# Kernel optimization log

Measured on AMD Instinct MI355X. Metric: run time of the kernel, lower is better.

The kernel has to match this reference:

```python
import jax, jax.numpy as jnp
import numpy as np
import math

B, S, HID = 2, 2048, 1024
NH, HD = 16, 64  # num_heads, head_dim = HID // NH


def setup_inputs() -> dict:
    key = jax.random.key(0)
    ks = jax.random.split(key, 12)
    sc = 1.0 / math.sqrt(HID)
    inp = {
        "x": jax.random.normal(ks[0], (B, S, HID), dtype=jnp.float32),
        "time_deltas": jax.random.uniform(ks[1], (B, S), dtype=jnp.float32),
        # torch.nn.Linear weights are [out, in]; y = x @ W.T + b
        "Wq": jax.random.normal(ks[2], (HID, HID), dtype=jnp.float32) * sc,
        "bq": jnp.zeros((HID,), dtype=jnp.float32),
        "Wk": jax.random.normal(ks[3], (HID, HID), dtype=jnp.float32) * sc,
        "bk": jnp.zeros((HID,), dtype=jnp.float32),
        "Wv": jax.random.normal(ks[4], (HID, HID), dtype=jnp.float32) * sc,
        "bv": jnp.zeros((HID,), dtype=jnp.float32),
        "Wo": jax.random.normal(ks[5], (HID, HID), dtype=jnp.float32) * sc,
        "bo": jnp.zeros((HID,), dtype=jnp.float32),
        "time_decay": jnp.ones((NH,), dtype=jnp.float32),
    }
    return inp


def reference(x, time_deltas, Wq, bq, Wk, bk, Wv, bv, Wo, bo, time_decay):
    b, s, _ = x.shape

    def heads(W, bias):
        # [b, s, hid] -> [b, nh, s, hd]
        return (x @ W.T + bias).reshape(b, s, NH, HD).transpose(0, 2, 1, 3)

    q = heads(Wq, bq)
    k = heads(Wk, bk)
    v = heads(Wv, bv)

    scores = jnp.einsum("bhqd,bhkd->bhqk", q, k) / math.sqrt(HD)

    # pairwise |t_i - t_j| decay bias, per-head learned rate
    tm = jnp.abs(time_deltas[:, :, None] - time_deltas[:, None, :])  # [b, s, s]
    decay = jnp.exp(-time_decay[None, :, None, None] * tm[:, None, :, :])
    scores = scores * decay

    causal = jnp.triu(jnp.ones((s, s), dtype=bool), k=1)  # True above diagonal
    scores = jnp.where(causal[None, None], -jnp.inf, scores)

    attn = jax.nn.softmax(scores, axis=-1)  # dropout is identity at inference
    out = jnp.einsum("bhqk,bhkd->bhqd", attn, v)
    out = out.transpose(0, 2, 1, 3).reshape(b, s, HID)
    return out @ Wo.T + bo
```

## Files before the change

### kernel.cpp

```cpp
#include <hip/hip_runtime.h>
#include <hip/hip_bf16.h>

typedef __attribute__((ext_vector_type(4))) float f32x4;
typedef __attribute__((ext_vector_type(8))) __bf16 bf16x8;
typedef __attribute__((ext_vector_type(4))) unsigned short us4;

static constexpr int BB = 2, SS = 2048, HID = 1024, NH = 16, HD = 64;
static constexpr int M_TOT = BB * SS;

static __device__ __forceinline__ f32x4 mfma16(bf16x8 a, bf16x8 b, f32x4 c) {
  return __builtin_amdgcn_mfma_f32_16x16x32_bf16(a, b, c, 0, 0, 0);
}

static __device__ __forceinline__ unsigned short f2b(float x) {
  __hip_bfloat16 h = __float2bfloat16(x);
  unsigned short u;
  __builtin_memcpy(&u, &h, 2);
  return u;
}

static __device__ __forceinline__ float ex2(float x) {
  return __builtin_amdgcn_exp2f(x);
}

__global__ void cvt_kernel(const float* __restrict__ src,
                           unsigned short* __restrict__ dst, int n4) {
  int idx = blockIdx.x * blockDim.x + threadIdx.x;
  int stride = gridDim.x * blockDim.x;
  const f32x4* s = (const f32x4*)src;
  us4* d = (us4*)dst;
  for (int i = idx; i < n4; i += stride) {
    f32x4 v = s[i];
    us4 o;
    o.x = f2b(v.x); o.y = f2b(v.y); o.z = f2b(v.z); o.w = f2b(v.w);
    d[i] = o;
  }
}

__global__ void cvt_w4(const float* __restrict__ s0, const float* __restrict__ s1,
                       const float* __restrict__ s2, const float* __restrict__ s3,
                       unsigned short* __restrict__ d0, unsigned short* __restrict__ d1,
                       unsigned short* __restrict__ d2, unsigned short* __restrict__ d3,
                       int n4) {
  const float* s; unsigned short* d;
  int z = blockIdx.y;
  if (z == 0)      { s = s0; d = d0; }
  else if (z == 1) { s = s1; d = d1; }
  else if (z == 2) { s = s2; d = d2; }
  else             { s = s3; d = d3; }
  int idx = blockIdx.x * blockDim.x + threadIdx.x;
  int stride = gridDim.x * blockDim.x;
  const f32x4* sv = (const f32x4*)s;
  us4* dv = (us4*)d;
  for (int i = idx; i < n4; i += stride) {
    f32x4 v = sv[i];
    us4 o;
    o.x = f2b(v.x); o.y = f2b(v.y); o.z = f2b(v.z); o.w = f2b(v.w);
    dv[i] = o;
  }
}

static __device__ __forceinline__ void gemm_mainloop(
    const unsigned short* __restrict__ gA,
    const unsigned short* __restrict__ gB,
    unsigned short* As, unsigned short* Bs, int t, f32x4 acc[4][4]) {
  const int l = t & 63;
  const int lr = l & 15, lg = (l >> 4) & 3;
  const int w = t >> 6;
  const int wr = w >> 1, wc = w & 1;
  for (int k0 = 0; k0 < HID; k0 += 64) {
#pragma unroll
    for (int i_ = 0; i_ < 4; ++i_) {
      int chunk = i_ * 256 + t;
      int row = chunk >> 3;
      int col = (chunk & 7) << 3;
      __builtin_amdgcn_global_load_lds(
          (const __attribute__((address_space(1))) unsigned int*)(gA + (size_t)row * HID + k0 + col),
          (__attribute__((address_space(3))) unsigned int*)(As + chunk * 8),
          16, 0, 0);
    }
#pragma unroll
    for (int i_ = 0; i_ < 4; ++i_) {
      int chunk = i_ * 256 + t;
      int row = chunk >> 3;
      int col = (chunk & 7) << 3;
      __builtin_amdgcn_global_load_lds(
          (const __attribute__((address_space(1))) unsigned int*)(gB + (size_t)row * HID + k0 + col),
          (__attribute__((address_space(3))) unsigned int*)(Bs + chunk * 8),
          16, 0, 0);
    }
    __syncthreads();
#pragma unroll
    for (int kk = 0; kk < 2; ++kk) {
      bf16x8 a[4], bb[4];
#pragma unroll
      for (int mf = 0; mf < 4; ++mf)
        a[mf] = *(const bf16x8*)&As[(wr * 64 + mf * 16 + lr) * 64 + kk * 32 + lg * 8];
#pragma unroll
      for (int nf = 0; nf < 4; ++nf)
        bb[nf] = *(const bf16x8*)&Bs[(wc * 64 + nf * 16 + lr) * 64 + kk * 32 + lg * 8];
#pragma unroll
      for (int mf = 0; mf < 4; ++mf)
#pragma unroll
        for (int nf = 0; nf < 4; ++nf)
          acc[mf][nf] = mfma16(a[mf], bb[nf], acc[mf][nf]);
    }
    __syncthreads();
  }
}

__global__ __launch_bounds__(256, 2) void qkv_gemm(
    const unsigned short* __restrict__ xb,
    const unsigned short* __restrict__ wqb, const unsigned short* __restrict__ wkb,
    const unsigned short* __restrict__ wvb,
    const float* __restrict__ bq, const float* __restrict__ bk, const float* __restrict__ bv,
    unsigned short* __restrict__ qo, unsigned short* __restrict__ ko,
    unsigned short* __restrict__ vto) {
  __shared__ unsigned short As[128 * 64];
  __shared__ unsigned short Bs[128 * 64];
  int t = threadIdx.x;
  int z = blockIdx.z;
  const unsigned short* Bmat = (z == 0) ? wqb : (z == 1) ? wkb : wvb;
  const float* bias = (z == 0) ? bq : (z == 1) ? bk : bv;
  int m0 = blockIdx.y * 128, n0 = blockIdx.x * 128;
  f32x4 acc[4][4] = {};
  gemm_mainloop(xb + (size_t)m0 * HID, Bmat + (size_t)n0 * HID, As, Bs, t, acc);

  int l = t & 63, lr = l & 15, lg = (l >> 4) & 3;
  int w = t >> 6, wr = w >> 1, wc = w & 1;
  float scale = (z == 0) ? 0.125f : 1.0f;
#pragma unroll
  for (int nf = 0; nf < 4; ++nf) {
    int n = n0 + wc * 64 + nf * 16 + lr;
    float bs = bias[n];
    int h = n >> 6, d = n & 63;
#pragma unroll
    for (int mf = 0; mf < 4; ++mf) {
#pragma unroll
      for (int j = 0; j < 4; ++j) {
        int m = m0 + wr * 64 + mf * 16 + lg * 4 + j;
        int b = m >> 11, sidx = m & (SS - 1);
        float val = (acc[mf][nf][j] + bs) * scale;
        unsigned short ob = f2b(val);
        if (z == 2)
          vto[((size_t)(b * NH + h) * HD + d) * SS + sidx] = ob;
        else {
          unsigned short* dst = (z == 0) ? qo : ko;
          dst[((size_t)(b * NH + h) * SS + sidx) * HD + d] = ob;
        }
      }
    }
  }
}

__global__ __launch_bounds__(256, 2) void out_gemm(
    const unsigned short* __restrict__ Ab,
    const unsigned short* __restrict__ Wb,
    const float* __restrict__ bias,
    float* __restrict__ C) {
  __shared__ unsigned short As[128 * 64];
  __shared__ unsigned short Bs[128 * 64];
  int t = threadIdx.x;
  int m0 = blockIdx.y * 128, n0 = blockIdx.x * 128;
  f32x4 acc[4][4] = {};
  gemm_mainloop(Ab + (size_t)m0 * HID, Wb + (size_t)n0 * HID, As, Bs, t, acc);

  int l = t & 63, lr = l & 15, lg = (l >> 4) & 3;
  int w = t >> 6, wr = w >> 1, wc = w & 1;
#pragma unroll
  for (int nf = 0; nf < 4; ++nf) {
    int n = n0 + wc * 64 + nf * 16 + lr;
    float bs = bias[n];
#pragma unroll
    for (int mf = 0; mf < 4; ++mf) {
#pragma unroll
      for (int j = 0; j < 4; ++j) {
        int m = m0 + wr * 64 + mf * 16 + lg * 4 + j;
        C[(size_t)m * HID + n] = acc[mf][nf][j] + bs;
      }
    }
  }
}

static __device__ __forceinline__ void stage_kv(
    const unsigned short* __restrict__ kp, const unsigned short* __restrict__ vp,
    int kv0, unsigned short* Kd, unsigned short* Vd, int t) {
#pragma unroll
  for (int i_ = 0; i_ < 2; ++i_) {
    int chunk = i_ * 256 + t;
    int row = chunk >> 3;
    int srcc = ((chunk & 7) ^ (row & 7)) << 3;
    __builtin_amdgcn_global_load_lds(
        (const __attribute__((address_space(1))) unsigned int*)(kp + (size_t)(kv0 + row) * HD + srcc),
        (__attribute__((address_space(3))) unsigned int*)(Kd + chunk * 8), 16, 0, 0);
    __builtin_amdgcn_global_load_lds(
        (const __attribute__((address_space(1))) unsigned int*)(vp + (size_t)row * SS + kv0 + srcc),
        (__attribute__((address_space(3))) unsigned int*)(Vd + chunk * 8), 16, 0, 0);
  }
}

__global__ __launch_bounds__(256, 2) void attn_kernel(
    const unsigned short* __restrict__ qg,
    const unsigned short* __restrict__ kg,
    const unsigned short* __restrict__ vtg,
    const float* __restrict__ td,
    const float* __restrict__ decay,
    unsigned short* __restrict__ outb) {
  __shared__ unsigned short Ks[2][64 * 64];
  __shared__ unsigned short Vs[2][64 * 64];
  __shared__ unsigned short Pl[4][16][64];
  const int t = threadIdx.x;
  const int l = t & 63;
  const int w = t >> 6;
  const int lr = l & 15, lg = (l >> 4) & 3;
  const int L = blockIdx.x;
  const int W = (L & 7) * 64 + (L >> 3);
  const int xp = W & 15;
  const int h = (W >> 4) & 15;
  const int b = W >> 8;
  const unsigned short* qp = qg + ((size_t)(b * NH + h) * SS) * HD;
  const unsigned short* kp = kg + ((size_t)(b * NH + h) * SS) * HD;
  const unsigned short* vp = vtg + ((size_t)(b * NH + h) * HD) * SS;
  const float* tdb = td + (size_t)b * SS;
  const float dec = decay[h];
  const float L2E = 1.44269504f;
  const float dl = dec * L2E;
  const float SHIFT = 16.0f;

  for (int seg = 0; seg < 2; ++seg) {
    const int qb = seg ? 31 - xp : xp;
    const int q0 = qb * 64;
    const int qw = q0 + w * 16;

    bf16x8 qf0 = *(const bf16x8*)&qp[(size_t)(qw + lr) * HD + lg * 8];
    bf16x8 qf1 = *(const bf16x8*)&qp[(size_t)(qw + lr) * HD + 32 + lg * 8];
    float eqL[4], fqL[4];
#pragma unroll
    for (int j = 0; j < 4; ++j) {
      float tq = tdb[qw + lg * 4 + j];
      eqL[j] = ex2(dl * tq) * L2E;
      fqL[j] = ex2(-dl * tq) * L2E;
    }
    float lsum[4] = {0.f, 0.f, 0.f, 0.f};
    f32x4 o[4] = {};

    stage_kv(kp, vp, 0, Ks[0], Vs[0], t);
    int cur = 0;
    for (int tkv = 0; tkv <= qb; ++tkv) {
      const int kv0 = tkv * 64;
      if (tkv < qb) {
        stage_kv(kp, vp, kv0 + 64, Ks[cur ^ 1], Vs[cur ^ 1], t);
        asm volatile("s_waitcnt vmcnt(4)" ::: "memory");
      } else {
        asm volatile("s_waitcnt vmcnt(0)" ::: "memory");
      }
      __builtin_amdgcn_s_barrier();
      asm volatile("" ::: "memory");
      const unsigned short* Kc = Ks[cur];
      const unsigned short* Vc = Vs[cur];

      f32x4 s[4];
#pragma unroll
      for (int nf = 0; nf < 4; ++nf) {
        int r = nf * 16 + lr;
        bf16x8 kf0 = *(const bf16x8*)&Kc[r * 64 + ((lg ^ (r & 7)) << 3)];
        bf16x8 kf1 = *(const bf16x8*)&Kc[r * 64 + (((4 + lg) ^ (r & 7)) << 3)];
        f32x4 zz = {};
        zz = mfma16(qf0, kf0, zz);
        s[nf] = mfma16(qf1, kf1, zz);
      }
      const bool diag = (tkv == qb);
#pragma unroll
      for (int nf = 0; nf < 4; ++nf) {
        int col = kv0 + nf * 16 + lr;
        float tk = tdb[col];
        float ek = ex2(dl * tk);
        float fk = ex2(-dl * tk);
#pragma unroll
        for (int j = 0; j < 4; ++j) {
          int row = lg * 4 + j;
          float wL = fminf(eqL[j] * fk, fqL[j] * ek);
          float pv = ex2(s[nf][j] * wL - SHIFT);
          if (diag && col > qw + row) pv = 0.f;
          lsum[j] += pv;
          Pl[w][row][(nf * 16 + lr) ^ ((row & 7) << 3)] = f2b(pv);
        }
      }
#pragma unroll
      for (int kk = 0; kk < 2; ++kk) {
        bf16x8 pa = *(const bf16x8*)&Pl[w][lr][(kk * 32 + lg * 8) ^ ((lr & 7) << 3)];
        int g = kk * 4 + lg;
#pragma unroll
        for (int df = 0; df < 4; ++df) {
          int r = df * 16 + lr;
          bf16x8 vf = *(const bf16x8*)&Vc[r * 64 + ((g ^ (r & 7)) << 3)];
          o[df] = mfma16(pa, vf, o[df]);
        }
      }
      __syncthreads();
      cur ^= 1;
    }
#pragma unroll
    for (int j = 0; j < 4; ++j) {
      float rs = lsum[j];
      rs += __shfl_xor(rs, 1, 16);
      rs += __shfl_xor(rs, 2, 16);
      rs += __shfl_xor(rs, 4, 16);
      rs += __shfl_xor(rs, 8, 16);
      float inv = 1.0f / rs;
      int srow = qw + lg * 4 + j;
#pragma unroll
      for (int df = 0; df < 4; ++df)
        outb[((size_t)b * SS + srow) * HID + h * HD + df * 16 + lr] = f2b(o[df][j] * inv);
    }
  }
}

extern "C" void kernel_launch(void* const* d_in, const int* in_sizes, int n_in,
                              void* d_out, int out_size, void* d_ws, size_t ws_size,
                              hipStream_t stream) {
  const float* x    = (const float*)d_in[0];
  const float* td   = (const float*)d_in[1];
  const float* Wq   = (const float*)d_in[2];
  const float* bq   = (const float*)d_in[3];
  const float* Wk   = (const float*)d_in[4];
  const float* bk   = (const float*)d_in[5];
  const float* Wv   = (const float*)d_in[6];
  const float* bv   = (const float*)d_in[7];
  const float* Wo   = (const float*)d_in[8];
  const float* bo   = (const float*)d_in[9];
  const float* tdec = (const float*)d_in[10];
  float* out = (float*)d_out;

  char* ws = (char*)d_ws;
  unsigned short* xb  = (unsigned short*)ws; ws += (size_t)M_TOT * HID * 2;
  unsigned short* wqb = (unsigned short*)ws; ws += (size_t)HID * HID * 2;
  unsigned short* wkb = (unsigned short*)ws; ws += (size_t)HID * HID * 2;
  unsigned short* wvb = (unsigned short*)ws; ws += (size_t)HID * HID * 2;
  unsigned short* wob = (unsigned short*)ws; ws += (size_t)HID * HID * 2;
  unsigned short* qb  = (unsigned short*)ws; ws += (size_t)M_TOT * HID * 2;
  unsigned short* kb  = (unsigned short*)ws; ws += (size_t)M_TOT * HID * 2;
  unsigned short* vtb = (unsigned short*)ws; ws += (size_t)M_TOT * HID * 2;
  unsigned short* ob  = (unsigned short*)ws; ws += (size_t)M_TOT * HID * 2;

  cvt_kernel<<<1024, 256, 0, stream>>>(x, xb, M_TOT * HID / 4);
  cvt_w4<<<dim3(512, 4), 256, 0, stream>>>(Wq, Wk, Wv, Wo, wqb, wkb, wvb, wob, HID * HID / 4);
  qkv_gemm<<<dim3(HID / 128, M_TOT / 128, 3), 256, 0, stream>>>(
      xb, wqb, wkb, wvb, bq, bk, bv, qb, kb, vtb);
  attn_kernel<<<512, 256, 0, stream>>>(qb, kb, vtb, td, tdec, ob);
  out_gemm<<<dim3(HID / 128, M_TOT / 128), 256, 0, stream>>>(ob, wob, bo, out);
}
```

Measured before the change: 210.8 us.

## Double-buffer GEMM LDS tiles and merge conversion kernels into one launch

The shared GEMM mainloop now prefetches the next K tile into a second LDS buffer via global_load_lds while computing on the current one, using explicit vmcnt waits and raw barriers instead of __syncthreads. LDS per block doubles to 64 KB, which may limit occupancy for the two-blocks-per-CU launch bound. The separate x and weight fp32-to-bf16 conversion kernels are merged into a single launch with a 5-row grid to save one kernel launch. The x slice now gets 512 blocks instead of 1024, so the larger conversion has less parallelism.

After: 227.6 us. +8.0%, slower.

```diff
diff --git a/kernel.cpp b/kernel.cpp
--- a/kernel.cpp
+++ b/kernel.cpp
@@ -23,31 +23,19 @@
   return __builtin_amdgcn_exp2f(x);
 }
 
-__global__ void cvt_kernel(const float* __restrict__ src,
-                           unsigned short* __restrict__ dst, int n4) {
-  int idx = blockIdx.x * blockDim.x + threadIdx.x;
-  int stride = gridDim.x * blockDim.x;
-  const f32x4* s = (const f32x4*)src;
-  us4* d = (us4*)dst;
-  for (int i = idx; i < n4; i += stride) {
-    f32x4 v = s[i];
-    us4 o;
-    o.x = f2b(v.x); o.y = f2b(v.y); o.z = f2b(v.z); o.w = f2b(v.w);
-    d[i] = o;
-  }
-}
-
-__global__ void cvt_w4(const float* __restrict__ s0, const float* __restrict__ s1,
-                       const float* __restrict__ s2, const float* __restrict__ s3,
-                       unsigned short* __restrict__ d0, unsigned short* __restrict__ d1,
-                       unsigned short* __restrict__ d2, unsigned short* __restrict__ d3,
-                       int n4) {
-  const float* s; unsigned short* d;
-  int z = blockIdx.y;
-  if (z == 0)      { s = s0; d = d0; }
-  else if (z == 1) { s = s1; d = d1; }
-  else if (z == 2) { s = s2; d = d2; }
-  else             { s = s3; d = d3; }
+__global__ void cvt_all(const float* __restrict__ x,  const float* __restrict__ wq,
+                        const float* __restrict__ wk, const float* __restrict__ wv,
+                        const float* __restrict__ wo,
+                        unsigned short* __restrict__ xb,  unsigned short* __restrict__ wqb,
+                        unsigned short* __restrict__ wkb, unsigned short* __restrict__ wvb,
+                        unsigned short* __restrict__ wob) {
+  int y = blockIdx.y;
+  const float* s; unsigned short* d; int n4;
+  if (y == 0)      { s = x;  d = xb;  n4 = M_TOT * HID / 4; }
+  else if (y == 1) { s = wq; d = wqb; n4 = HID * HID / 4; }
+  else if (y == 2) { s = wk; d = wkb; n4 = HID * HID / 4; }
+  else if (y == 3) { s = wv; d = wvb; n4 = HID * HID / 4; }
+  else             { s = wo; d = wob; n4 = HID * HID / 4; }
   int idx = blockIdx.x * blockDim.x + threadIdx.x;
   int stride = gridDim.x * blockDim.x;
   const f32x4* sv = (const f32x4*)s;
@@ -60,52 +48,63 @@
   }
 }
 
+static __device__ __forceinline__ void stage_ab(
+    const unsigned short* __restrict__ gA, const unsigned short* __restrict__ gB,
+    int k0, unsigned short* As, unsigned short* Bs, int t) {
+#pragma unroll
+  for (int i_ = 0; i_ < 4; ++i_) {
+    int chunk = i_ * 256 + t;
+    int row = chunk >> 3;
+    int col = (chunk & 7) << 3;
+    __builtin_amdgcn_global_load_lds(
+        (const __attribute__((address_space(1))) unsigned int*)(gA + (size_t)row * HID + k0 + col),
+        (__attribute__((address_space(3))) unsigned int*)(As + chunk * 8), 16, 0, 0);
+    __builtin_amdgcn_global_load_lds(
+        (const __attribute__((address_space(1))) unsigned int*)(gB + (size_t)row * HID + k0 + col),
+        (__attribute__((address_space(3))) unsigned int*)(Bs + chunk * 8), 16, 0, 0);
+  }
+}
+
 static __device__ __forceinline__ void gemm_mainloop(
     const unsigned short* __restrict__ gA,
     const unsigned short* __restrict__ gB,
-    unsigned short* As, unsigned short* Bs, int t, f32x4 acc[4][4]) {
+    unsigned short* As, unsigned short* Bs,
+    int t, f32x4 acc[4][4]) {
   const int l = t & 63;
   const int lr = l & 15, lg = (l >> 4) & 3;
   const int w = t >> 6;
   const int wr = w >> 1, wc = w & 1;
+  stage_ab(gA, gB, 0, As, Bs, t);
+  int cur = 0;
   for (int k0 = 0; k0 < HID; k0 += 64) {
-#pragma unroll
-    for (int i_ = 0; i_ < 4; ++i_) {
-      int chunk = i_ * 256 + t;
-      int row = chunk >> 3;
-      int col = (chunk & 7) << 3;
-      __builtin_amdgcn_global_load_lds(
-          (const __attribute__((address_space(1))) unsigned int*)(gA + (size_t)row * HID + k0 + col),
-          (__attribute__((address_space(3))) unsigned int*)(As + chunk * 8),
-          16, 0, 0);
-    }
-#pragma unroll
-    for (int i_ = 0; i_ < 4; ++i_) {
-      int chunk = i_ * 256 + t;
-      int row = chunk >> 3;
-      int col = (chunk & 7) << 3;
-      __builtin_amdgcn_global_load_lds(
-          (const __attribute__((address_space(1))) unsigned int*)(gB + (size_t)row * HID + k0 + col),
-          (__attribute__((address_space(3))) unsigned int*)(Bs + chunk * 8),
-          16, 0, 0);
-    }
-    __syncthreads();
+    if (k0 + 64 < HID) {
+      stage_ab(gA, gB, k0 + 64, As + (cur ^ 1) * 8192, Bs + (cur ^ 1) * 8192, t);
+      asm volatile("s_waitcnt vmcnt(8)" ::: "memory");
+    } else {
+      asm volatile("s_waitcnt vmcnt(0)" ::: "memory");
+    }
+    __builtin_amdgcn_s_barrier();
+    asm volatile("" ::: "memory");
+    const unsigned short* Ac = As + cur * 8192;
+    const unsigned short* Bc = Bs + cur * 8192;
 #pragma unroll
     for (int kk = 0; kk < 2; ++kk) {
       bf16x8 a[4], bb[4];
 #pragma unroll
       for (int mf = 0; mf < 4; ++mf)
-        a[mf] = *(const bf16x8*)&As[(wr * 64 + mf * 16 + lr) * 64 + kk * 32 + lg * 8];
+        a[mf] = *(const bf16x8*)&Ac[(wr * 64 + mf * 16 + lr) * 64 + kk * 32 + lg * 8];
 #pragma unroll
       for (int nf = 0; nf < 4; ++nf)
-        bb[nf] = *(const bf16x8*)&Bs[(wc * 64 + nf * 16 + lr) * 64 + kk * 32 + lg * 8];
+        bb[nf] = *(const bf16x8*)&Bc[(wc * 64 + nf * 16 + lr) * 64 + kk * 32 + lg * 8];
 #pragma unroll
       for (int mf = 0; mf < 4; ++mf)
 #pragma unroll
         for (int nf = 0; nf < 4; ++nf)
           acc[mf][nf] = mfma16(a[mf], bb[nf], acc[mf][nf]);
     }
-    __syncthreads();
+    asm volatile("" ::: "memory");
+    __builtin_amdgcn_s_barrier();
+    cur ^= 1;
   }
 }
 
@@ -116,8 +115,8 @@
     const float* __restrict__ bq, const float* __restrict__ bk, const float* __restrict__ bv,
     unsigned short* __restrict__ qo, unsigned short* __restrict__ ko,
     unsigned short* __restrict__ vto) {
-  __shared__ unsigned short As[128 * 64];
-  __shared__ unsigned short Bs[128 * 64];
+  __shared__ unsigned short As[2 * 128 * 64];
+  __shared__ unsigned short Bs[2 * 128 * 64];
   int t = threadIdx.x;
   int z = blockIdx.z;
   const unsigned short* Bmat = (z == 0) ? wqb : (z == 1) ? wkb : wvb;
@@ -158,8 +157,8 @@
     const unsigned short* __restrict__ Wb,
     const float* __restrict__ bias,
     float* __restrict__ C) {
-  __shared__ unsigned short As[128 * 64];
-  __shared__ unsigned short Bs[128 * 64];
+  __shared__ unsigned short As[2 * 128 * 64];
+  __shared__ unsigned short Bs[2 * 128 * 64];
   int t = threadIdx.x;
   int m0 = blockIdx.y * 128, n0 = blockIdx.x * 128;
   f32x4 acc[4][4] = {};
@@ -343,8 +342,7 @@
   unsigned short* vtb = (unsigned short*)ws; ws += (size_t)M_TOT * HID * 2;
   unsigned short* ob  = (unsigned short*)ws; ws += (size_t)M_TOT * HID * 2;
 
-  cvt_kernel<<<1024, 256, 0, stream>>>(x, xb, M_TOT * HID / 4);
-  cvt_w4<<<dim3(512, 4), 256, 0, stream>>>(Wq, Wk, Wv, Wo, wqb, wkb, wvb, wob, HID * HID / 4);
+  cvt_all<<<dim3(512, 5), 256, 0, stream>>>(x, Wq, Wk, Wv, Wo, xb, wqb, wkb, wvb, wob);
   qkv_gemm<<<dim3(HID / 128, M_TOT / 128, 3), 256, 0, stream>>>(
       xb, wqb, wkb, wvb, bq, bk, bv, qb, kb, vtb);
   attn_kernel<<<512, 256, 0, stream>>>(qb, kb, vtb, td, tdec, ob);
```
